# Kernel tuning notes

Hardware: AMD Instinct MI355X
Metric: run time of the kernel (lower is better)

## Reference

```python
import jax, jax.numpy as jnp
import numpy as np

N_NODES = 20000
N_EDGES = 320000
HIDDEN = 64
M = 8            # extra per-node sample axis implied by Linear2's (N, B, M) layout
IN_DIM = 1
OUT_DIM = 1
N_LAYERS = 5
BN_EPS = 1e-5


def setup_inputs() -> dict:
    key = jax.random.key(0)
    ks = jax.random.split(key, 10)
    x = jax.random.normal(ks[0], (N_NODES, IN_DIM, M), dtype=jnp.float32)
    edge_index = jax.random.randint(ks[1], (2, N_EDGES), 0, N_NODES, dtype=jnp.int64)
    batch = jnp.zeros((N_NODES,), dtype=jnp.int64)
    s = 0.1
    w1_0 = jax.random.normal(ks[2], (HIDDEN, IN_DIM), dtype=jnp.float32) * s
    w1 = jax.random.normal(ks[3], (N_LAYERS - 1, HIDDEN, HIDDEN), dtype=jnp.float32) * s
    b1 = jax.random.normal(ks[4], (N_LAYERS, HIDDEN), dtype=jnp.float32) * s
    w2 = jax.random.normal(ks[5], (N_LAYERS, HIDDEN, HIDDEN), dtype=jnp.float32) * s
    b2 = jax.random.normal(ks[6], (N_LAYERS, HIDDEN), dtype=jnp.float32) * s
    gamma = jnp.ones((N_LAYERS, HIDDEN), dtype=jnp.float32)
    beta = jnp.zeros((N_LAYERS, HIDDEN), dtype=jnp.float32)
    w_out = jax.random.normal(ks[7], (OUT_DIM, HIDDEN), dtype=jnp.float32) * s
    b_out = jnp.zeros((OUT_DIM,), dtype=jnp.float32)
    return {"x": x, "edge_index": edge_index, "batch": batch,
            "w1_0": w1_0, "w1": w1, "b1": b1, "w2": w2, "b2": b2,
            "gamma": gamma, "beta": beta, "w_out": w_out, "b_out": b_out}


def reference(x, edge_index, batch, w1_0, w1, b1, w2, b2, gamma, beta, w_out, b_out):
    src, dst = edge_index[0], edge_index[1]
    n = x.shape[0]
    h = x  # [N, C, M]
    for i in range(N_LAYERS):
        # GINConv (eps=0): nn(x + sum of neighbor features scattered by dst)
        agg = jax.ops.segment_sum(h[src], dst, num_segments=n)
        z = h + agg
        W1 = w1_0 if i == 0 else w1[i - 1]
        # Linear2 applies the linear over the channel axis (axis 1)
        z = jnp.einsum('ncm,oc->nom', z, W1) + b1[i][None, :, None]
        z = jax.nn.relu(z)
        z = jnp.einsum('ncm,oc->nom', z, w2[i]) + b2[i][None, :, None]
        z = jax.nn.relu(z)
        # BatchNorm1d over (N, C, M): per-channel stats over N and M (training-mode batch stats)
        mean = z.mean(axis=(0, 2), keepdims=True)
        var = z.var(axis=(0, 2), keepdims=True)
        z = (z - mean) * jax.lax.rsqrt(var + BN_EPS)
        z = z * gamma[i][None, :, None] + beta[i][None, :, None]
        # Dropout(0.5) treated as identity (eval behavior, deterministic reference)
        h = z
    # global mean pool with batch of all zeros -> single graph
    pooled = h.mean(axis=0, keepdims=True)          # [1, H, M]
    pooled = jnp.transpose(pooled, (0, 2, 1))        # [1, M, H]
    out = jax.nn.sigmoid(jnp.einsum('bmh,oh->bmo', pooled, w_out) + b_out)
    return out  # [1, M, OUT_DIM]
```

## Files before the change

### kernel.cpp

```cpp
#include <hip/hip_runtime.h>

#define N_NODES 20000
#define N_EDGES 320000
#define HID 64
#define MDIM 8
#define ROW 512
#define NM 160000.0f
#define NCHUNK 79
#define NSHADOW 16
#define ZSTRIDE 72

typedef unsigned int uint;
typedef unsigned char uchar;
typedef unsigned short ushort;
typedef __attribute__((ext_vector_type(8))) short bf16x8;
typedef __attribute__((ext_vector_type(4))) float f32x4;
typedef __attribute__((ext_vector_type(2))) float f32x2;

union U4B8 { uint4 u; bf16x8 b; };

__device__ __forceinline__ float bflo(uint u) { return __uint_as_float(u << 16); }
__device__ __forceinline__ float bfhi(uint u) { return __uint_as_float(u & 0xffff0000u); }
__device__ __forceinline__ uint f2bf(float f) {
    uint u = __float_as_uint(f);
    return (u + 0x7fffu + ((u >> 16) & 1u)) >> 16;
}
__device__ __forceinline__ uint pack2(float lo, float hi) { return f2bf(lo) | (f2bf(hi) << 16); }
__device__ __forceinline__ uint2 pkfp8(uint4 pk) {
    int lo = 0, hi = 0;
    lo = __builtin_amdgcn_cvt_pk_fp8_f32(bflo(pk.x), bfhi(pk.x), lo, false);
    lo = __builtin_amdgcn_cvt_pk_fp8_f32(bflo(pk.y), bfhi(pk.y), lo, true);
    hi = __builtin_amdgcn_cvt_pk_fp8_f32(bflo(pk.z), bfhi(pk.z), hi, false);
    hi = __builtin_amdgcn_cvt_pk_fp8_f32(bflo(pk.w), bfhi(pk.w), hi, true);
    uint2 r; r.x = (uint)lo; r.y = (uint)hi; return r;
}

__global__ __launch_bounds__(256) void k_hist(const int* __restrict__ dst, int* __restrict__ deg) {
    int e = blockIdx.x * 256 + threadIdx.x;
    if (e < N_EDGES) atomicAdd(&deg[dst[e]], 1);
}

__global__ __launch_bounds__(256) void k_csum(const int* __restrict__ deg, int* __restrict__ csum) {
    __shared__ int r[256];
    int t = threadIdx.x, i = blockIdx.x * 256 + t;
    r[t] = (i < N_NODES) ? deg[i] : 0;
    __syncthreads();
    for (int s = 128; s > 0; s >>= 1) { if (t < s) r[t] += r[t + s]; __syncthreads(); }
    if (t == 0) csum[blockIdx.x] = r[0];
}

__global__ __launch_bounds__(128) void k_cscan(const int* __restrict__ csum, int* __restrict__ chunkoff) {
    __shared__ int s[128];
    int t = threadIdx.x;
    s[t] = (t < NCHUNK) ? csum[t] : 0;
    __syncthreads();
    if (t == 0) { int run = 0; for (int j = 0; j < NCHUNK; ++j) { int x = s[j]; s[j] = run; run += x; } }
    __syncthreads();
    if (t < NCHUNK) chunkoff[t] = s[t];
}

__global__ __launch_bounds__(256) void k_chunkscan(const int* __restrict__ deg, const int* __restrict__ chunkoff,
                                                   int* __restrict__ offs) {
    __shared__ int sd[256];
    int t = threadIdx.x, i = blockIdx.x * 256 + t;
    int v = (i < N_NODES) ? deg[i] : 0;
    sd[t] = v;
    __syncthreads();
    for (int off = 1; off < 256; off <<= 1) {
        int x = (t >= off) ? sd[t - off] : 0;
        __syncthreads();
        sd[t] += x;
        __syncthreads();
    }
    if (i < N_NODES) offs[i] = sd[t] - v + chunkoff[blockIdx.x];
}

__global__ __launch_bounds__(256) void k_fill(const int* __restrict__ src, const int* __restrict__ dst,
                                              const int* __restrict__ offs, int* __restrict__ cursor,
                                              int* __restrict__ esrc) {
    int e = blockIdx.x * 256 + threadIdx.x;
    if (e < N_EDGES) {
        int d = dst[e];
        int p = atomicAdd(&cursor[d], 1);
        esrc[offs[d] + p] = src[e];
    }
}

__global__ __launch_bounds__(256) void k_prep(const float* __restrict__ w1, const float* __restrict__ w2,
                                              uint4* __restrict__ wfrag) {
    int id = blockIdx.x * 256 + threadIdx.x;
    if (id >= 4608) return;
    const float* W;
    int s;
    if (id < 4096) {
        int layer = id >> 10;
        int rem = id & 1023;
        int which = rem >> 9;
        s = rem & 511;
        W = which ? &w2[(size_t)(layer + 1) * 4096] : &w1[(size_t)layer * 4096];
    } else {
        s = id - 4096;
        W = w2;
    }
    int f = s >> 6, l = s & 63;
    int o = (f >> 1) * 16 + (l & 15);
    int c0 = (f & 1) * 32 + (l >> 4) * 8;
    const float* p = &W[o * 64 + c0];
    uint4 a;
    a.x = pack2(p[0], p[1]); a.y = pack2(p[2], p[3]);
    a.z = pack2(p[4], p[5]); a.w = pack2(p[6], p[7]);
    wfrag[id] = a;
}

__global__ __launch_bounds__(256) void k_layer0(const float* __restrict__ x, const int* __restrict__ offs,
                                                const int* __restrict__ deg, const int* __restrict__ esrc,
                                                const float* __restrict__ W10, const float* __restrict__ B1,
                                                const uint4* __restrict__ w2f0, const float* __restrict__ B2,
                                                uchar* __restrict__ zout8, float* __restrict__ shadow) {
    __shared__ uint4 w2s[512];
    __shared__ __align__(16) ushort zbuf[128 * ZSTRIDE];
    int tid = threadIdx.x;
    for (int s2 = tid; s2 < 512; s2 += 256) w2s[s2] = w2f0[s2];
    __syncthreads();
    int w = tid >> 6, t = tid & 63;
    int n0 = blockIdx.x * 16 + w * 4;
    int g = t >> 3, m = t & 7;
    float zin0v[4];
    #pragma unroll
    for (int i = 0; i < 4; ++i) {
        int n = n0 + i;
        int off = offs[n], dg = deg[n];
        float acc = (t < 8) ? x[n * 8 + t] : 0.f;
        for (int base = 0; base < dg; base += 8) {
            int k = base + g;
            float v = 0.f;
            if (k < dg) { int nb = esrc[off + k]; v = x[(size_t)nb * 8 + m]; }
            acc += v;
        }
        acc += __shfl_xor(acc, 8);
        acc += __shfl_xor(acc, 16);
        acc += __shfl_xor(acc, 32);
        zin0v[i] = acc;
    }
    bf16x8 bfr[2][2];
    #pragma unroll
    for (int q2 = 0; q2 < 2; ++q2) {
        int kb = q2 * 32 + (t >> 4) * 8;
        float4 wA = *(const float4*)&W10[kb];
        float4 wB = *(const float4*)&W10[kb + 4];
        float4 bA = *(const float4*)&B1[kb];
        float4 bB = *(const float4*)&B1[kb + 4];
        #pragma unroll
        for (int tau = 0; tau < 2; ++tau) {
            float zv = zin0v[tau * 2 + ((t & 15) >> 3)];
            U4B8 u;
            u.u.x = pack2(fmaxf(fmaf(wA.x, zv, bA.x), 0.f), fmaxf(fmaf(wA.y, zv, bA.y), 0.f));
            u.u.y = pack2(fmaxf(fmaf(wA.z, zv, bA.z), 0.f), fmaxf(fmaf(wA.w, zv, bA.w), 0.f));
            u.u.z = pack2(fmaxf(fmaf(wB.x, zv, bB.x), 0.f), fmaxf(fmaf(wB.y, zv, bB.y), 0.f));
            u.u.w = pack2(fmaxf(fmaf(wB.z, zv, bB.z), 0.f), fmaxf(fmaf(wB.w, zv, bB.w), 0.f));
            bfr[q2][tau] = u.b;
        }
    }
    f32x4 acc[4][2];
    #pragma unroll
    for (int o4 = 0; o4 < 4; ++o4) {
        float4 bv = *(const float4*)&B2[o4 * 16 + (t >> 4) * 4];
        #pragma unroll
        for (int tau = 0; tau < 2; ++tau) acc[o4][tau] = (f32x4){bv.x, bv.y, bv.z, bv.w};
    }
    #pragma unroll
    for (int o4 = 0; o4 < 4; ++o4)
        #pragma unroll
        for (int q2 = 0; q2 < 2; ++q2) {
            U4B8 a; a.u = w2s[(o4 * 2 + q2) * 64 + t];
            #pragma unroll
            for (int tau = 0; tau < 2; ++tau)
                acc[o4][tau] = __builtin_amdgcn_mfma_f32_16x16x32_bf16(a.b, bfr[q2][tau], acc[o4][tau], 0, 0, 0);
        }
    #pragma unroll
    for (int o4 = 0; o4 < 4; ++o4)
        #pragma unroll
        for (int tau = 0; tau < 2; ++tau) {
            acc[o4][tau][0] = fmaxf(acc[o4][tau][0], 0.f);
            acc[o4][tau][1] = fmaxf(acc[o4][tau][1], 0.f);
            acc[o4][tau][2] = fmaxf(acc[o4][tau][2], 0.f);
            acc[o4][tau][3] = fmaxf(acc[o4][tau][3], 0.f);
        }
    int sid = (blockIdx.x & (NSHADOW - 1)) * 128;
    #pragma unroll
    for (int o4 = 0; o4 < 4; ++o4)
        #pragma unroll
        for (int r = 0; r < 4; ++r) {
            float x0 = acc[o4][0][r], x1 = acc[o4][1][r];
            float sv = x0 + x1;
            float ssv = x0 * x0 + x1 * x1;
            sv += __shfl_xor(sv, 1);  ssv += __shfl_xor(ssv, 1);
            sv += __shfl_xor(sv, 2);  ssv += __shfl_xor(ssv, 2);
            sv += __shfl_xor(sv, 4);  ssv += __shfl_xor(ssv, 4);
            sv += __shfl_xor(sv, 8);  ssv += __shfl_xor(ssv, 8);
            if ((t & 15) == o4 * 4 + r) {
                int ch = o4 * 16 + (t >> 4) * 4 + r;
                atomicAdd(&shadow[sid + ch], sv);
                atomicAdd(&shadow[sid + 64 + ch], ssv);
            }
        }
    #pragma unroll
    for (int o4 = 0; o4 < 4; ++o4)
        #pragma unroll
        for (int tau = 0; tau < 2; ++tau) {
            uint* p = (uint*)&zbuf[(w * 32 + tau * 16 + (t & 15)) * ZSTRIDE + o4 * 16 + (t >> 4) * 4];
            p[0] = pack2(acc[o4][tau][0], acc[o4][tau][1]);
            p[1] = pack2(acc[o4][tau][2], acc[o4][tau][3]);
        }
    #pragma unroll
    for (int i = 0; i < 4; ++i) {
        uint4 pk = *(const uint4*)&zbuf[(w * 32 + i * 8 + (t >> 3)) * ZSTRIDE + (t & 7) * 8];
        ((uint2*)(zout8 + (size_t)(n0 + i) * ROW))[t] = pkfp8(pk);
    }
}

__global__ __launch_bounds__(256) void k_layer(const uchar* __restrict__ zprev8,
                                               const float* __restrict__ shadow_prev,
                                               const float* __restrict__ gammaP, const float* __restrict__ betaP,
                                               const int* __restrict__ offs, const int* __restrict__ deg,
                                               const int* __restrict__ esrc,
                                               const uint4* __restrict__ w1f, const float* __restrict__ B1,
                                               const uint4* __restrict__ w2f, const float* __restrict__ B2,
                                               uchar* __restrict__ zout8, float* __restrict__ shadow) {
    __shared__ uint4 w1s[512];
    __shared__ uint4 w2s[512];
    __shared__ __align__(16) ushort zbuf[128 * ZSTRIDE];
    __shared__ float red[128];
    __shared__ __align__(16) float abl[128];
    int tid = threadIdx.x;
    for (int s2 = tid; s2 < 512; s2 += 256) { w1s[s2] = w1f[s2]; w2s[s2] = w2f[s2]; }
    if (tid < 128) {
        float s = 0.f;
        #pragma unroll
        for (int j = 0; j < NSHADOW; ++j) s += shadow_prev[j * 128 + tid];
        red[tid] = s;
    }
    __syncthreads();
    if (tid < 64) {
        float mean = red[tid] * (1.f / NM);
        float var = red[64 + tid] * (1.f / NM) - mean * mean;
        float a = gammaP[tid] * rsqrtf(var + 1e-5f);
        abl[tid] = a;
        abl[64 + tid] = betaP[tid] - mean * a;
    }
    __syncthreads();
    int w = tid >> 6, t = tid & 63;
    int n0 = blockIdx.x * 16 + w * 4;
    const float4* abp = (const float4*)abl;
    float4 Alo = abp[(t & 7) * 2], Ahi = abp[(t & 7) * 2 + 1];
    float4 Blo = abp[16 + (t & 7) * 2], Bhi = abp[16 + (t & 7) * 2 + 1];
    for (int i = 0; i < 4; ++i) {
        int n = n0 + i;
        int off = offs[n], dg = deg[n];
        uint2 sv = ((const uint2*)(zprev8 + (size_t)n * ROW))[t];
        f32x2 s0 = __builtin_amdgcn_cvt_pk_f32_fp8((int)sv.x, false);
        f32x2 s1 = __builtin_amdgcn_cvt_pk_f32_fp8((int)sv.x, true);
        f32x2 s2 = __builtin_amdgcn_cvt_pk_f32_fp8((int)sv.y, false);
        f32x2 s3 = __builtin_amdgcn_cvt_pk_f32_fp8((int)sv.y, true);
        float a0 = s0.x, a1 = s0.y, a2 = s1.x, a3 = s1.y;
        float a4 = s2.x, a5 = s2.y, a6 = s3.x, a7 = s3.y;
        for (int base = 0; base < dg; base += 64) {
            int rem = dg - base;
            int cnt = rem < 64 ? rem : 64;
            int idx = (t < cnt) ? esrc[off + base + t] : 0;
            int j = 0;
            for (; j + 3 < cnt; j += 4) {
                int nb0 = __builtin_amdgcn_readlane(idx, j);
                int nb1 = __builtin_amdgcn_readlane(idx, j + 1);
                int nb2 = __builtin_amdgcn_readlane(idx, j + 2);
                int nb3 = __builtin_amdgcn_readlane(idx, j + 3);
                uint2 r0 = ((const uint2*)(zprev8 + (size_t)nb0 * ROW))[t];
                uint2 r1 = ((const uint2*)(zprev8 + (size_t)nb1 * ROW))[t];
                uint2 r2 = ((const uint2*)(zprev8 + (size_t)nb2 * ROW))[t];
                uint2 r3 = ((const uint2*)(zprev8 + (size_t)nb3 * ROW))[t];
                f32x2 p0, p1, p2, p3;
                p0 = __builtin_amdgcn_cvt_pk_f32_fp8((int)r0.x, false);
                p1 = __builtin_amdgcn_cvt_pk_f32_fp8((int)r0.x, true);
                p2 = __builtin_amdgcn_cvt_pk_f32_fp8((int)r0.y, false);
                p3 = __builtin_amdgcn_cvt_pk_f32_fp8((int)r0.y, true);
                a0 += p0.x; a1 += p0.y; a2 += p1.x; a3 += p1.y;
                a4 += p2.x; a5 += p2.y; a6 += p3.x; a7 += p3.y;
                p0 = __builtin_amdgcn_cvt_pk_f32_fp8((int)r1.x, false);
                p1 = __builtin_amdgcn_cvt_pk_f32_fp8((int)r1.x, true);
                p2 = __builtin_amdgcn_cvt_pk_f32_fp8((int)r1.y, false);
                p3 = __builtin_amdgcn_cvt_pk_f32_fp8((int)r1.y, true);
                a0 += p0.x; a1 += p0.y; a2 += p1.x; a3 += p1.y;
                a4 += p2.x; a5 += p2.y; a6 += p3.x; a7 += p3.y;
                p0 = __builtin_amdgcn_cvt_pk_f32_fp8((int)r2.x, false);
                p1 = __builtin_amdgcn_cvt_pk_f32_fp8((int)r2.x, true);
                p2 = __builtin_amdgcn_cvt_pk_f32_fp8((int)r2.y, false);
                p3 = __builtin_amdgcn_cvt_pk_f32_fp8((int)r2.y, true);
                a0 += p0.x; a1 += p0.y; a2 += p1.x; a3 += p1.y;
                a4 += p2.x; a5 += p2.y; a6 += p3.x; a7 += p3.y;
                p0 = __builtin_amdgcn_cvt_pk_f32_fp8((int)r3.x, false);
                p1 = __builtin_amdgcn_cvt_pk_f32_fp8((int)r3.x, true);
                p2 = __builtin_amdgcn_cvt_pk_f32_fp8((int)r3.y, false);
                p3 = __builtin_amdgcn_cvt_pk_f32_fp8((int)r3.y, true);
                a0 += p0.x; a1 += p0.y; a2 += p1.x; a3 += p1.y;
                a4 += p2.x; a5 += p2.y; a6 += p3.x; a7 += p3.y;
            }
            for (; j < cnt; ++j) {
                int nb = __builtin_amdgcn_readlane(idx, j);
                uint2 r = ((const uint2*)(zprev8 + (size_t)nb * ROW))[t];
                f32x2 p0 = __builtin_amdgcn_cvt_pk_f32_fp8((int)r.x, false);
                f32x2 p1 = __builtin_amdgcn_cvt_pk_f32_fp8((int)r.x, true);
                f32x2 p2 = __builtin_amdgcn_cvt_pk_f32_fp8((int)r.y, false);
                f32x2 p3 = __builtin_amdgcn_cvt_pk_f32_fp8((int)r.y, true);
                a0 += p0.x; a1 += p0.y; a2 += p1.x; a3 += p1.y;
                a4 += p2.x; a5 += p2.y; a6 += p3.x; a7 += p3.y;
            }
        }
        float dp1 = (float)(dg + 1);
        uint4 pk;
        pk.x = pack2(fmaf(Alo.x, a0, Blo.x * dp1), fmaf(Alo.y, a1, Blo.y * dp1));
        pk.y = pack2(fmaf(Alo.z, a2, Blo.z * dp1), fmaf(Alo.w, a3, Blo.w * dp1));
        pk.z = pack2(fmaf(Ahi.x, a4, Bhi.x * dp1), fmaf(Ahi.y, a5, Bhi.y * dp1));
        pk.w = pack2(fmaf(Ahi.z, a6, Bhi.z * dp1), fmaf(Ahi.w, a7, Bhi.w * dp1));
        *(uint4*)&zbuf[(w * 32 + i * 8 + (t >> 3)) * ZSTRIDE + (t & 7) * 8] = pk;
    }
    bf16x8 bfr[2][2];
    #pragma unroll
    for (int tau = 0; tau < 2; ++tau)
        #pragma unroll
        for (int q2 = 0; q2 < 2; ++q2) {
            U4B8 u;
            u.u = *(const uint4*)&zbuf[(w * 32 + tau * 16 + (t & 15)) * ZSTRIDE + q2 * 32 + (t >> 4) * 8];
            bfr[q2][tau] = u.b;
        }
    f32x4 acc[4][2];
    #pragma unroll
    for (int o4 = 0; o4 < 4; ++o4) {
        float4 bv = *(const float4*)&B1[o4 * 16 + (t >> 4) * 4];
        #pragma unroll
        for (int tau = 0; tau < 2; ++tau) acc[o4][tau] = (f32x4){bv.x, bv.y, bv.z, bv.w};
    }
    #pragma unroll
    for (int o4 = 0; o4 < 4; ++o4)
        #pragma unroll
        for (int q2 = 0; q2 < 2; ++q2) {
            U4B8 a; a.u = w1s[(o4 * 2 + q2) * 64 + t];
            #pragma unroll
            for (int tau = 0; tau < 2; ++tau)
                acc[o4][tau] = __builtin_amdgcn_mfma_f32_16x16x32_bf16(a.b, bfr[q2][tau], acc[o4][tau], 0, 0, 0);
        }
    #pragma unroll
    for (int o4 = 0; o4 < 4; ++o4)
        #pragma unroll
        for (int tau = 0; tau < 2; ++tau) {
            f32x4 v = acc[o4][tau];
            float h0 = fmaxf(v[0], 0.f), h1 = fmaxf(v[1], 0.f), h2 = fmaxf(v[2], 0.f), h3 = fmaxf(v[3], 0.f);
            uint* p = (uint*)&zbuf[(w * 32 + tau * 16 + (t & 15)) * ZSTRIDE + o4 * 16 + (t >> 4) * 4];
            p[0] = pack2(h0, h1); p[1] = pack2(h2, h3);
        }
    #pragma unroll
    for (int tau = 0; tau < 2; ++tau)
        #pragma unroll
        for (int q2 = 0; q2 < 2; ++q2) {
            U4B8 u;
            u.u = *(const uint4*)&zbuf[(w * 32 + tau * 16 + (t & 15)) * ZSTRIDE + q2 * 32 + (t >> 4) * 8];
            bfr[q2][tau] = u.b;
        }
    #pragma unroll
    for (int o4 = 0; o4 < 4; ++o4) {
        float4 bv = *(const float4*)&B2[o4 * 16 + (t >> 4) * 4];
        #pragma unroll
        for (int tau = 0; tau < 2; ++tau) acc[o4][tau] = (f32x4){bv.x, bv.y, bv.z, bv.w};
    }
    #pragma unroll
    for (int o4 = 0; o4 < 4; ++o4)
        #pragma unroll
        for (int q2 = 0; q2 < 2; ++q2) {
            U4B8 a; a.u = w2s[(o4 * 2 + q2) * 64 + t];
            #pragma unroll
            for (int tau = 0; tau < 2; ++tau)
                acc[o4][tau] = __builtin_amdgcn_mfma_f32_16x16x32_bf16(a.b, bfr[q2][tau], acc[o4][tau], 0, 0, 0);
        }
    #pragma unroll
    for (int o4 = 0; o4 < 4; ++o4)
        #pragma unroll
        for (int tau = 0; tau < 2; ++tau) {
            acc[o4][tau][0] = fmaxf(acc[o4][tau][0], 0.f);
            acc[o4][tau][1] = fmaxf(acc[o4][tau][1], 0.f);
            acc[o4][tau][2] = fmaxf(acc[o4][tau][2], 0.f);
            acc[o4][tau][3] = fmaxf(acc[o4][tau][3], 0.f);
        }
    int sid = (blockIdx.x & (NSHADOW - 1)) * 128;
    #pragma unroll
    for (int o4 = 0; o4 < 4; ++o4)
        #pragma unroll
        for (int r = 0; r < 4; ++r) {
            float x0 = acc[o4][0][r], x1 = acc[o4][1][r];
            float sv = x0 + x1;
            float ssv = x0 * x0 + x1 * x1;
            sv += __shfl_xor(sv, 1);  ssv += __shfl_xor(ssv, 1);
            sv += __shfl_xor(sv, 2);  ssv += __shfl_xor(ssv, 2);
            sv += __shfl_xor(sv, 4);  ssv += __shfl_xor(ssv, 4);
            sv += __shfl_xor(sv, 8);  ssv += __shfl_xor(ssv, 8);
            if ((t & 15) == o4 * 4 + r) {
                int ch = o4 * 16 + (t >> 4) * 4 + r;
                atomicAdd(&shadow[sid + ch], sv);
                atomicAdd(&shadow[sid + 64 + ch], ssv);
            }
        }
    #pragma unroll
    for (int o4 = 0; o4 < 4; ++o4)
        #pragma unroll
        for (int tau = 0; tau < 2; ++tau) {
            uint* p = (uint*)&zbuf[(w * 32 + tau * 16 + (t & 15)) * ZSTRIDE + o4 * 16 + (t >> 4) * 4];
            p[0] = pack2(acc[o4][tau][0], acc[o4][tau][1]);
            p[1] = pack2(acc[o4][tau][2], acc[o4][tau][3]);
        }
    #pragma unroll
    for (int i = 0; i < 4; ++i) {
        uint4 pk = *(const uint4*)&zbuf[(w * 32 + i * 8 + (t >> 3)) * ZSTRIDE + (t & 7) * 8];
        ((uint2*)(zout8 + (size_t)(n0 + i) * ROW))[t] = pkfp8(pk);
    }
}

__global__ __launch_bounds__(256) void k_pool(const uint* __restrict__ z8, float* __restrict__ pool) {
    int t = blockIdx.x * 256 + threadIdx.x;
    float s0 = 0.f, s1 = 0.f, s2 = 0.f, s3 = 0.f;
    for (int u = t; u < N_NODES * ROW / 4; u += 65536) {
        uint v = z8[u];
        f32x2 p0 = __builtin_amdgcn_cvt_pk_f32_fp8((int)v, false);
        f32x2 p1 = __builtin_amdgcn_cvt_pk_f32_fp8((int)v, true);
        s0 += p0.x; s1 += p0.y; s2 += p1.x; s3 += p1.y;
    }
    int k4 = t & 127;
    atomicAdd(&pool[k4 * 4 + 0], s0);
    atomicAdd(&pool[k4 * 4 + 1], s1);
    atomicAdd(&pool[k4 * 4 + 2], s2);
    atomicAdd(&pool[k4 * 4 + 3], s3);
}

__global__ __launch_bounds__(64) void k_out(const float* __restrict__ pool, const float* __restrict__ shadow4,
                                            const float* __restrict__ gamma4, const float* __restrict__ beta4,
                                            const float* __restrict__ wout, const float* __restrict__ bout,
                                            float* __restrict__ out) {
    int c = threadIdx.x;
    float s = 0.f, ss = 0.f;
    #pragma unroll
    for (int j = 0; j < NSHADOW; ++j) { s += shadow4[j * 128 + c]; ss += shadow4[j * 128 + 64 + c]; }
    float mean = s * (1.f / NM);
    float var = ss * (1.f / NM) - mean * mean;
    float a = gamma4[c] * rsqrtf(var + 1e-5f);
    float b = beta4[c] - mean * a;
    float wv = wout[c];
    for (int m = 0; m < 8; ++m) {
        float v = wv * (a * pool[m * 64 + c] * (1.f / N_NODES) + b);
        for (int off = 32; off > 0; off >>= 1) v += __shfl_down(v, off);
        if (c == 0) out[m] = 1.f / (1.f + expf(-(v + bout[0])));
    }
}

extern "C" void kernel_launch(void* const* d_in, const int* in_sizes, int n_in,
                              void* d_out, int out_size, void* d_ws, size_t ws_size,
                              hipStream_t stream) {
    const float* x     = (const float*)d_in[0];
    const int*   ei    = (const int*)d_in[1];
    const int*   srcp  = ei;
    const int*   dstp  = ei + N_EDGES;
    const float* w1_0  = (const float*)d_in[3];
    const float* w1    = (const float*)d_in[4];
    const float* b1    = (const float*)d_in[5];
    const float* w2    = (const float*)d_in[6];
    const float* b2    = (const float*)d_in[7];
    const float* gamma = (const float*)d_in[8];
    const float* beta  = (const float*)d_in[9];
    const float* wout  = (const float*)d_in[10];
    const float* bout  = (const float*)d_in[11];
    float* out = (float*)d_out;

    char* ws = (char*)d_ws;
    size_t off = 0;
    auto alloc = [&](size_t bytes) -> void* {
        void* p = ws + off;
        off = (off + bytes + 255) & ~(size_t)255;
        return p;
    };
    uchar* zA8   = (uchar*)alloc((size_t)N_NODES * ROW);
    uchar* zB8   = (uchar*)alloc((size_t)N_NODES * ROW);
    uint4* wfrag = (uint4*)alloc(4608 * 16);
    int* deg      = (int*)alloc(N_NODES * 4);
    int* cursor   = (int*)alloc(N_NODES * 4);
    float* shadow = (float*)alloc(5 * NSHADOW * 128 * 4);
    float* pool   = (float*)alloc(512 * 4);
    size_t zero_bytes = (size_t)((char*)pool - (char*)deg) + 512 * 4;
    int* offs     = (int*)alloc(N_NODES * 4);
    int* esrc     = (int*)alloc(N_EDGES * 4);
    int* csum     = (int*)alloc(NCHUNK * 4);
    int* chunkoff = (int*)alloc(NCHUNK * 4);

    hipMemsetAsync(deg, 0, zero_bytes, stream);

    k_hist<<<(N_EDGES + 255) / 256, 256, 0, stream>>>(dstp, deg);
    k_csum<<<NCHUNK, 256, 0, stream>>>(deg, csum);
    k_cscan<<<1, 128, 0, stream>>>(csum, chunkoff);
    k_chunkscan<<<NCHUNK, 256, 0, stream>>>(deg, chunkoff, offs);
    k_fill<<<(N_EDGES + 255) / 256, 256, 0, stream>>>(srcp, dstp, offs, cursor, esrc);
    k_prep<<<18, 256, 0, stream>>>(w1, w2, wfrag);

    k_layer0<<<N_NODES / 16, 256, 0, stream>>>(x, offs, deg, esrc, w1_0, b1, wfrag + 4096, b2,
                                               zA8, shadow);

    const uchar* zin8 = zA8;
    uchar* zo8 = zB8;
    for (int i = 1; i <= 4; ++i) {
        k_layer<<<N_NODES / 16, 256, 0, stream>>>(zin8,
                                                  shadow + (size_t)(i - 1) * NSHADOW * 128,
                                                  gamma + (i - 1) * 64, beta + (i - 1) * 64,
                                                  offs, deg, esrc,
                                                  wfrag + (size_t)(i - 1) * 1024, b1 + i * 64,
                                                  wfrag + (size_t)(i - 1) * 1024 + 512, b2 + i * 64,
                                                  zo8,
                                                  shadow + (size_t)i * NSHADOW * 128);
        const uchar* t8 = zin8; zin8 = zo8; zo8 = (uchar*)t8;
    }

    k_pool<<<256, 256, 0, stream>>>((const uint*)zA8, pool);
    k_out<<<1, 64, 0, stream>>>(pool, shadow + 4 * NSHADOW * 128, gamma + 256, beta + 256, wout, bout, out);
}
```

Before: 483.7 us.

## Gather two neighbor rows per wave with 16-byte loads and drop weight LDS staging

The neighbor gather now splits each wave into two half-waves that each fetch a different neighbor's full 512-byte fp8 row with uint4 loads. This doubles the bytes per load instruction and halves the loop trip count, and the two partial sums are combined with a cross-half shuffle. Edge offsets, degrees and the first 64 source indices are prefetched before the BN-stat barrier to hide their latency. MFMA weight fragments are read directly from global memory instead of being staged in LDS, which frees 16KB of shared memory per block and may raise occupancy. The cost is more accumulator registers and extra shuffle work.

```diff
diff --git a/kernel.cpp b/kernel.cpp
--- a/kernel.cpp
+++ b/kernel.cpp
@@ -219,6 +219,25 @@
     }
 }
 
+#define PAIRLD(rr, jj) do { \
+    int nb_l = __builtin_amdgcn_readlane(idx, (jj)); \
+    int nb_h = __builtin_amdgcn_readlane(idx, (jj) + 1); \
+    int nb_ = hi ? nb_h : nb_l; \
+    rr = ((const uint4*)(zprev8 + (size_t)nb_ * ROW))[q]; \
+} while (0)
+
+#define ACC16(rr) do { \
+    f32x2 p_; \
+    p_ = __builtin_amdgcn_cvt_pk_f32_fp8((int)rr.x, false); s0  += p_.x; s1  += p_.y; \
+    p_ = __builtin_amdgcn_cvt_pk_f32_fp8((int)rr.x, true);  s2  += p_.x; s3  += p_.y; \
+    p_ = __builtin_amdgcn_cvt_pk_f32_fp8((int)rr.y, false); s4  += p_.x; s5  += p_.y; \
+    p_ = __builtin_amdgcn_cvt_pk_f32_fp8((int)rr.y, true);  s6  += p_.x; s7  += p_.y; \
+    p_ = __builtin_amdgcn_cvt_pk_f32_fp8((int)rr.z, false); s8  += p_.x; s9  += p_.y; \
+    p_ = __builtin_amdgcn_cvt_pk_f32_fp8((int)rr.z, true);  s10 += p_.x; s11 += p_.y; \
+    p_ = __builtin_amdgcn_cvt_pk_f32_fp8((int)rr.w, false); s12 += p_.x; s13 += p_.y; \
+    p_ = __builtin_amdgcn_cvt_pk_f32_fp8((int)rr.w, true);  s14 += p_.x; s15 += p_.y; \
+} while (0)
+
 __global__ __launch_bounds__(256) void k_layer(const uchar* __restrict__ zprev8,
                                                const float* __restrict__ shadow_prev,
                                                const float* __restrict__ gammaP, const float* __restrict__ betaP,
@@ -227,13 +246,19 @@
                                                const uint4* __restrict__ w1f, const float* __restrict__ B1,
                                                const uint4* __restrict__ w2f, const float* __restrict__ B2,
                                                uchar* __restrict__ zout8, float* __restrict__ shadow) {
-    __shared__ uint4 w1s[512];
-    __shared__ uint4 w2s[512];
     __shared__ __align__(16) ushort zbuf[128 * ZSTRIDE];
     __shared__ float red[128];
     __shared__ __align__(16) float abl[128];
     int tid = threadIdx.x;
-    for (int s2 = tid; s2 < 512; s2 += 256) { w1s[s2] = w1f[s2]; w2s[s2] = w2f[s2]; }
+    int w = tid >> 6, t = tid & 63;
+    int n0 = blockIdx.x * 16 + w * 4;
+    int q = t & 31;
+    int hi = t >> 5;
+    int offv[4], dgv[4], idxv[4];
+    #pragma unroll
+    for (int i = 0; i < 4; ++i) { offv[i] = offs[n0 + i]; dgv[i] = deg[n0 + i]; }
+    #pragma unroll
+    for (int i = 0; i < 4; ++i) idxv[i] = (t < dgv[i]) ? esrc[offv[i] + t] : 0;
     if (tid < 128) {
         float s = 0.f;
         #pragma unroll
@@ -249,79 +274,62 @@
         abl[64 + tid] = betaP[tid] - mean * a;
     }
     __syncthreads();
-    int w = tid >> 6, t = tid & 63;
-    int n0 = blockIdx.x * 16 + w * 4;
     const float4* abp = (const float4*)abl;
-    float4 Alo = abp[(t & 7) * 2], Ahi = abp[(t & 7) * 2 + 1];
-    float4 Blo = abp[16 + (t & 7) * 2], Bhi = abp[16 + (t & 7) * 2 + 1];
+    #pragma unroll
     for (int i = 0; i < 4; ++i) {
         int n = n0 + i;
-        int off = offs[n], dg = deg[n];
-        uint2 sv = ((const uint2*)(zprev8 + (size_t)n * ROW))[t];
-        f32x2 s0 = __builtin_amdgcn_cvt_pk_f32_fp8((int)sv.x, false);
-        f32x2 s1 = __builtin_amdgcn_cvt_pk_f32_fp8((int)sv.x, true);
-        f32x2 s2 = __builtin_amdgcn_cvt_pk_f32_fp8((int)sv.y, false);
-        f32x2 s3 = __builtin_amdgcn_cvt_pk_f32_fp8((int)sv.y, true);
-        float a0 = s0.x, a1 = s0.y, a2 = s1.x, a3 = s1.y;
-        float a4 = s2.x, a5 = s2.y, a6 = s3.x, a7 = s3.y;
+        int off = offv[i], dg = dgv[i];
+        float s0 = 0.f, s1 = 0.f, s2 = 0.f, s3 = 0.f, s4 = 0.f, s5 = 0.f, s6 = 0.f, s7 = 0.f;
+        float s8 = 0.f, s9 = 0.f, s10 = 0.f, s11 = 0.f, s12 = 0.f, s13 = 0.f, s14 = 0.f, s15 = 0.f;
         for (int base = 0; base < dg; base += 64) {
-            int rem = dg - base;
-            int cnt = rem < 64 ? rem : 64;
-            int idx = (t < cnt) ? esrc[off + base + t] : 0;
+            int cnt = dg - base; if (cnt > 64) cnt = 64;
+            int idx = base ? ((t < cnt) ? esrc[off + base + t] : 0) : idxv[i];
             int j = 0;
-            for (; j + 3 < cnt; j += 4) {
-                int nb0 = __builtin_amdgcn_readlane(idx, j);
-                int nb1 = __builtin_amdgcn_readlane(idx, j + 1);
-                int nb2 = __builtin_amdgcn_readlane(idx, j + 2);
-                int nb3 = __builtin_amdgcn_readlane(idx, j + 3);
-                uint2 r0 = ((const uint2*)(zprev8 + (size_t)nb0 * ROW))[t];
-                uint2 r1 = ((const uint2*)(zprev8 + (size_t)nb1 * ROW))[t];
-                uint2 r2 = ((const uint2*)(zprev8 + (size_t)nb2 * ROW))[t];
-                uint2 r3 = ((const uint2*)(zprev8 + (size_t)nb3 * ROW))[t];
-                f32x2 p0, p1, p2, p3;
-                p0 = __builtin_amdgcn_cvt_pk_f32_fp8((int)r0.x, false);
-                p1 = __builtin_amdgcn_cvt_pk_f32_fp8((int)r0.x, true);
-                p2 = __builtin_amdgcn_cvt_pk_f32_fp8((int)r0.y, false);
-                p3 = __builtin_amdgcn_cvt_pk_f32_fp8((int)r0.y, true);
-                a0 += p0.x; a1 += p0.y; a2 += p1.x; a3 += p1.y;
-                a4 += p2.x; a5 += p2.y; a6 += p3.x; a7 += p3.y;
-                p0 = __builtin_amdgcn_cvt_pk_f32_fp8((int)r1.x, false);
-                p1 = __builtin_amdgcn_cvt_pk_f32_fp8((int)r1.x, true);
-                p2 = __builtin_amdgcn_cvt_pk_f32_fp8((int)r1.y, false);
-                p3 = __builtin_amdgcn_cvt_pk_f32_fp8((int)r1.y, true);
-                a0 += p0.x; a1 += p0.y; a2 += p1.x; a3 += p1.y;
-                a4 += p2.x; a5 += p2.y; a6 += p3.x; a7 += p3.y;
-                p0 = __builtin_amdgcn_cvt_pk_f32_fp8((int)r2.x, false);
-                p1 = __builtin_amdgcn_cvt_pk_f32_fp8((int)r2.x, true);
-                p2 = __builtin_amdgcn_cvt_pk_f32_fp8((int)r2.y, false);
-                p3 = __builtin_amdgcn_cvt_pk_f32_fp8((int)r2.y, true);
-                a0 += p0.x; a1 += p0.y; a2 += p1.x; a3 += p1.y;
-                a4 += p2.x; a5 += p2.y; a6 += p3.x; a7 += p3.y;
-                p0 = __builtin_amdgcn_cvt_pk_f32_fp8((int)r3.x, false);
-                p1 = __builtin_amdgcn_cvt_pk_f32_fp8((int)r3.x, true);
-                p2 = __builtin_amdgcn_cvt_pk_f32_fp8((int)r3.y, false);
-                p3 = __builtin_amdgcn_cvt_pk_f32_fp8((int)r3.y, true);
-                a0 += p0.x; a1 += p0.y; a2 += p1.x; a3 += p1.y;
-                a4 += p2.x; a5 += p2.y; a6 += p3.x; a7 += p3.y;
+            for (; j + 7 < cnt; j += 8) {
+                uint4 r0, r1, r2, r3;
+                PAIRLD(r0, j); PAIRLD(r1, j + 2); PAIRLD(r2, j + 4); PAIRLD(r3, j + 6);
+                ACC16(r0); ACC16(r1); ACC16(r2); ACC16(r3);
             }
-            for (; j < cnt; ++j) {
+            for (; j + 1 < cnt; j += 2) {
+                uint4 r0;
+                PAIRLD(r0, j);
+                ACC16(r0);
+            }
+            if (j < cnt) {
                 int nb = __builtin_amdgcn_readlane(idx, j);
-                uint2 r = ((const uint2*)(zprev8 + (size_t)nb * ROW))[t];
-                f32x2 p0 = __builtin_amdgcn_cvt_pk_f32_fp8((int)r.x, false);
-                f32x2 p1 = __builtin_amdgcn_cvt_pk_f32_fp8((int)r.x, true);
-                f32x2 p2 = __builtin_amdgcn_cvt_pk_f32_fp8((int)r.y, false);
-                f32x2 p3 = __builtin_amdgcn_cvt_pk_f32_fp8((int)r.y, true);
-                a0 += p0.x; a1 += p0.y; a2 += p1.x; a3 += p1.y;
-                a4 += p2.x; a5 += p2.y; a6 += p3.x; a7 += p3.y;
+                if (!hi) {
+                    uint4 r0 = ((const uint4*)(zprev8 + (size_t)nb * ROW))[q];
+                    ACC16(r0);
+                }
             }
         }
+        float u, r0, r1, r2, r3, r4, r5, r6, r7;
+        u = hi ? s0 : s8;   r0 = (hi ? s8  : s0) + __shfl_xor(u, 32);
+        u = hi ? s1 : s9;   r1 = (hi ? s9  : s1) + __shfl_xor(u, 32);
+        u = hi ? s2 : s10;  r2 = (hi ? s10 : s2) + __shfl_xor(u, 32);
+        u = hi ? s3 : s11;  r3 = (hi ? s11 : s3) + __shfl_xor(u, 32);
+        u = hi ? s4 : s12;  r4 = (hi ? s12 : s4) + __shfl_xor(u, 32);
+        u = hi ? s5 : s13;  r5 = (hi ? s13 : s5) + __shfl_xor(u, 32);
+        u = hi ? s6 : s14;  r6 = (hi ? s14 : s6) + __shfl_xor(u, 32);
+        u = hi ? s7 : s15;  r7 = (hi ? s15 : s7) + __shfl_xor(u, 32);
+        {
+            uint2 sv = ((const uint2*)(zprev8 + (size_t)n * ROW))[q * 2 + hi];
+            f32x2 p_;
+            p_ = __builtin_amdgcn_cvt_pk_f32_fp8((int)sv.x, false); r0 += p_.x; r1 += p_.y;
+            p_ = __builtin_amdgcn_cvt_pk_f32_fp8((int)sv.x, true);  r2 += p_.x; r3 += p_.y;
+            p_ = __builtin_amdgcn_cvt_pk_f32_fp8((int)sv.y, false); r4 += p_.x; r5 += p_.y;
+            p_ = __builtin_amdgcn_cvt_pk_f32_fp8((int)sv.y, true);  r6 += p_.x; r7 += p_.y;
+        }
+        int c4 = (q & 3) * 4 + hi * 2;
+        float4 Af0 = abp[c4], Af1 = abp[c4 + 1];
+        float4 Bf0 = abp[16 + c4], Bf1 = abp[16 + c4 + 1];
         float dp1 = (float)(dg + 1);
         uint4 pk;
-        pk.x = pack2(fmaf(Alo.x, a0, Blo.x * dp1), fmaf(Alo.y, a1, Blo.y * dp1));
-        pk.y = pack2(fmaf(Alo.z, a2, Blo.z * dp1), fmaf(Alo.w, a3, Blo.w * dp1));
-        pk.z = pack2(fmaf(Ahi.x, a4, Bhi.x * dp1), fmaf(Ahi.y, a5, Bhi.y * dp1));
-        pk.w = pack2(fmaf(Ahi.z, a6, Bhi.z * dp1), fmaf(Ahi.w, a7, Bhi.w * dp1));
-        *(uint4*)&zbuf[(w * 32 + i * 8 + (t >> 3)) * ZSTRIDE + (t & 7) * 8] = pk;
+        pk.x = pack2(fmaf(Af0.x, r0, Bf0.x * dp1), fmaf(Af0.y, r1, Bf0.y * dp1));
+        pk.y = pack2(fmaf(Af0.z, r2, Bf0.z * dp1), fmaf(Af0.w, r3, Bf0.w * dp1));
+        pk.z = pack2(fmaf(Af1.x, r4, Bf1.x * dp1), fmaf(Af1.y, r5, Bf1.y * dp1));
+        pk.w = pack2(fmaf(Af1.z, r6, Bf1.z * dp1), fmaf(Af1.w, r7, Bf1.w * dp1));
+        *(uint4*)&zbuf[(w * 32 + i * 8 + (q >> 2)) * ZSTRIDE + (q & 3) * 16 + hi * 8] = pk;
     }
     bf16x8 bfr[2][2];
     #pragma unroll
@@ -343,7 +351,7 @@
     for (int o4 = 0; o4 < 4; ++o4)
         #pragma unroll
         for (int q2 = 0; q2 < 2; ++q2) {
-            U4B8 a; a.u = w1s[(o4 * 2 + q2) * 64 + t];
+            U4B8 a; a.u = w1f[(o4 * 2 + q2) * 64 + t];
             #pragma unroll
             for (int tau = 0; tau < 2; ++tau)
                 acc[o4][tau] = __builtin_amdgcn_mfma_f32_16x16x32_bf16(a.b, bfr[q2][tau], acc[o4][tau], 0, 0, 0);
@@ -375,7 +383,7 @@
     for (int o4 = 0; o4 < 4; ++o4)
         #pragma unroll
         for (int q2 = 0; q2 < 2; ++q2) {
-            U4B8 a; a.u = w2s[(o4 * 2 + q2) * 64 + t];
+            U4B8 a; a.u = w2f[(o4 * 2 + q2) * 64 + t];
             #pragma unroll
             for (int tau = 0; tau < 2; ++tau)
                 acc[o4][tau] = __builtin_amdgcn_mfma_f32_16x16x32_bf16(a.b, bfr[q2][tau], acc[o4][tau], 0, 0, 0);
```

Measured after the change: 492.6 us. About the same (+1.9%).
